# Optimization experiments

Hardware: AMD Instinct MI355X
Metric: run time of the kernel (lower is better)

The kernel has to match this reference:

```python
import jax, jax.numpy as jnp
import numpy as np

N_NODES = 100000
N_EDGES = 1600000
DIM = 64
LAYERS = 2


def setup_inputs() -> dict:
    key = jax.random.key(0)
    k1, k2, k3, k4 = jax.random.split(key, 4)
    h = jax.random.normal(k1, (N_NODES, DIM), dtype=jnp.float32)
    w = jax.random.uniform(k2, (N_EDGES,), dtype=jnp.float32)
    src = jax.random.randint(k3, (N_EDGES,), 0, N_NODES, dtype=jnp.int32)
    dst = jax.random.randint(k4, (N_EDGES,), 0, N_NODES, dtype=jnp.int32)
    return {"h": h, "w": w, "src": src, "dst": dst}


def reference(h, w, src, dst):
    N = h.shape[0]
    # weighted in-degree, clamped at 1 (DGL in_degrees(weight='w').clamp(min=1))
    deg = jnp.maximum(jax.ops.segment_sum(w, dst, num_segments=N), 1.0)
    norm = deg[:, None] ** -0.5  # [N, 1]
    embs = [h]
    for _ in range(LAYERS):
        h_norm = h * norm                              # [N, d]
        m = h_norm[src] * w[:, None]                   # [E, d] edge messages (u_mul_e)
        neigh_sum = jax.ops.segment_sum(m, dst, num_segments=N)  # fn.sum
        h = neigh_sum * norm
        embs.append(h)
    # mean over [h0, h1, ..., hL]
    return jnp.mean(jnp.stack(embs, axis=1), axis=1)
```

## Files before the change

kernel.cpp:

```cpp
#include <hip/hip_runtime.h>
#include <hip/hip_bf16.h>

#define D 64
#define THREADS 256
#define P2T 1024
#define BKT_BITS 9
#define BKT_NODES (1 << BKT_BITS)
#define CHUNK 2048

__device__ __forceinline__ unsigned f2bf(float f) {
    unsigned u = __float_as_uint(f);
    return (u + 0x7fffu + ((u >> 16) & 1u)) >> 16;
}
__device__ __forceinline__ float2 bfpair(unsigned v) {
    return make_float2(__uint_as_float(v << 16), __uint_as_float(v & 0xffff0000u));
}

typedef float f32x4 __attribute__((ext_vector_type(4)));
typedef unsigned u32x4 __attribute__((ext_vector_type(4)));
__device__ __forceinline__ void stnt_f4(float4 v, float4* p) {
    f32x4 t = {v.x, v.y, v.z, v.w};
    __builtin_nontemporal_store(t, (f32x4*)p);
}
__device__ __forceinline__ void stnt_u4(uint4 v, uint4* p) {
    u32x4 t = {v.x, v.y, v.z, v.w};
    __builtin_nontemporal_store(t, (u32x4*)p);
}

__global__ void p1a_hist(const int* __restrict__ dst, int* __restrict__ blockCount,
                         const float* __restrict__ h, unsigned* __restrict__ hbf2,
                         long long nd4, int E, int B) {
    __shared__ int lc[256];
    int t = threadIdx.x;
    lc[t] = 0;
    __syncthreads();
    for (long long i = (long long)blockIdx.x * THREADS + t; i < nd4;
         i += (long long)gridDim.x * THREADS) {
        float4 v = ((const float4*)h)[i];
        ((uint2*)hbf2)[i] = make_uint2(f2bf(v.x) | (f2bf(v.y) << 16),
                                       f2bf(v.z) | (f2bf(v.w) << 16));
    }
    int base = blockIdx.x * CHUNK;
    int end = min(base + CHUNK, E);
    int end4 = end >> 2;
    for (int e4 = (base >> 2) + t; e4 < end4; e4 += THREADS) {
        int4 d4 = ((const int4*)dst)[e4];
        atomicAdd(&lc[d4.x >> BKT_BITS], 1);
        atomicAdd(&lc[d4.y >> BKT_BITS], 1);
        atomicAdd(&lc[d4.z >> BKT_BITS], 1);
        atomicAdd(&lc[d4.w >> BKT_BITS], 1);
    }
    for (int e = (end4 << 2) + t; e < end; e += THREADS)
        atomicAdd(&lc[dst[e] >> BKT_BITS], 1);
    __syncthreads();
    if (t < B) blockCount[(long long)blockIdx.x * B + t] = lc[t];
}

__global__ void p1b_scanblocks(int* __restrict__ blockCount, int* __restrict__ total,
                               int NBLK, int B) {
    __shared__ int sm[512];
    int b = blockIdx.x, t = threadIdx.x;
    int run = 0;
    for (int base = 0; base < NBLK; base += 512) {
        int i = base + t;
        int v = (i < NBLK) ? blockCount[(long long)i * B + b] : 0;
        sm[t] = v;
        __syncthreads();
        for (int off = 1; off < 512; off <<= 1) {
            int u = (t >= off) ? sm[t - off] : 0;
            __syncthreads();
            sm[t] += u;
            __syncthreads();
        }
        if (i < NBLK) blockCount[(long long)i * B + b] = run + sm[t] - v;
        run += sm[511];
        __syncthreads();
    }
    if (t == 0) total[b] = run;
}

__global__ void p1c_scanbuckets(const int* __restrict__ total, int* __restrict__ bstart,
                                int B, int E) {
    __shared__ int sm[256];
    int t = threadIdx.x;
    int run = 0;
    for (int base = 0; base < B; base += 256) {
        int i = base + t;
        int v = (i < B) ? total[i] : 0;
        sm[t] = v;
        __syncthreads();
        for (int off = 1; off < 256; off <<= 1) {
            int u = (t >= off) ? sm[t - off] : 0;
            __syncthreads();
            sm[t] += u;
            __syncthreads();
        }
        if (i < B) bstart[i] = run + sm[t] - v;
        run += sm[255];
        __syncthreads();
    }
    if (t == 0) bstart[B] = E;
}

__global__ void p1d_scatter(const int* __restrict__ dst, const int* __restrict__ src,
                            const float* __restrict__ w, const int* __restrict__ blockCount,
                            const int* __restrict__ bstart, int2* __restrict__ temp,
                            int E, int B) {
    __shared__ int cur[256];
    int t = threadIdx.x;
    if (t < B) cur[t] = bstart[t] + blockCount[(long long)blockIdx.x * B + t];
    __syncthreads();
    int base = blockIdx.x * CHUNK;
    int end = min(base + CHUNK, E);
    int end4 = end >> 2;
    for (int e4 = (base >> 2) + t; e4 < end4; e4 += THREADS) {
        int4 d4 = ((const int4*)dst)[e4];
        int4 s4 = ((const int4*)src)[e4];
        float4 w4 = ((const float4*)w)[e4];
        int pos;
        pos = atomicAdd(&cur[d4.x >> BKT_BITS], 1);
        temp[pos] = make_int2(s4.x | ((d4.x & (BKT_NODES - 1)) << 17), __float_as_int(w4.x));
        pos = atomicAdd(&cur[d4.y >> BKT_BITS], 1);
        temp[pos] = make_int2(s4.y | ((d4.y & (BKT_NODES - 1)) << 17), __float_as_int(w4.y));
        pos = atomicAdd(&cur[d4.z >> BKT_BITS], 1);
        temp[pos] = make_int2(s4.z | ((d4.z & (BKT_NODES - 1)) << 17), __float_as_int(w4.z));
        pos = atomicAdd(&cur[d4.w >> BKT_BITS], 1);
        temp[pos] = make_int2(s4.w | ((d4.w & (BKT_NODES - 1)) << 17), __float_as_int(w4.w));
    }
    for (int e = (end4 << 2) + t; e < end; e += THREADS) {
        int d = dst[e];
        int pos = atomicAdd(&cur[d >> BKT_BITS], 1);
        temp[pos] = make_int2(src[e] | ((d & (BKT_NODES - 1)) << 17), __float_as_int(w[e]));
    }
}

__global__ __launch_bounds__(P2T)
void p2_build(const int2* __restrict__ temp, const int* __restrict__ bstart,
              int2* __restrict__ packed, int* __restrict__ rowptr,
              float* __restrict__ norm, int N, int E, int B) {
    __shared__ int cnt[BKT_NODES];
    __shared__ float degs[BKT_NODES];
    __shared__ int cur[BKT_NODES];
    __shared__ int sm[BKT_NODES];
    int b = blockIdx.x, t = threadIdx.x;
    int ebeg = bstart[b], eend = bstart[b + 1];
    if (t < BKT_NODES) { cnt[t] = 0; degs[t] = 0.0f; }
    __syncthreads();
    for (int e = ebeg + t; e < eend; e += P2T) {
        int2 pk = temp[e];
        int dl = (pk.x >> 17) & (BKT_NODES - 1);
        atomicAdd(&cnt[dl], 1);
        atomicAdd(&degs[dl], __int_as_float(pk.y));
    }
    __syncthreads();
    int v0 = 0;
    if (t < BKT_NODES) { v0 = cnt[t]; sm[t] = v0; }
    __syncthreads();
    for (int off = 1; off < BKT_NODES; off <<= 1) {
        int u = (t >= off && t < BKT_NODES) ? sm[t - off] : 0;
        __syncthreads();
        if (t < BKT_NODES) sm[t] += u;
        __syncthreads();
    }
    int node0 = b << BKT_BITS;
    if (t < BKT_NODES) {
        cur[t] = sm[t] - v0;
        int node = node0 + t;
        if (node < N) {
            rowptr[node] = ebeg + cur[t];
            norm[node] = rsqrtf(fmaxf(degs[t], 1.0f));
        }
    }
    if (b == 0 && t == 0) rowptr[N] = E;
    __syncthreads();
    for (int e = ebeg + t; e < eend; e += P2T) {
        int2 pk = temp[e];
        int dl = (pk.x >> 17) & (BKT_NODES - 1);
        int pos = atomicAdd(&cur[dl], 1);
        packed[ebeg + pos] = make_int2(pk.x & 0x1ffff, pk.y);
    }
}

#define EDGE_FMA(r, c, A0, A1, A2, A3, A4, A5, A6, A7) do {            \
    float2 fa = bfpair((r).x), fb = bfpair((r).y);                      \
    float2 fc = bfpair((r).z), fd = bfpair((r).w);                      \
    A0 = fmaf(fa.x, (c), A0); A1 = fmaf(fa.y, (c), A1);                 \
    A2 = fmaf(fb.x, (c), A2); A3 = fmaf(fb.y, (c), A3);                 \
    A4 = fmaf(fc.x, (c), A4); A5 = fmaf(fc.y, (c), A5);                 \
    A6 = fmaf(fd.x, (c), A6); A7 = fmaf(fd.y, (c), A7); } while (0)

__global__ void gather1_kernel(const uint4* __restrict__ h_in, const int2* __restrict__ packed,
                               const int* __restrict__ rowptr, const float* __restrict__ norm,
                               uint4* __restrict__ h_out, int N) {
    int node = blockIdx.x * (blockDim.x >> 3) + (threadIdx.x >> 3);
    int lane = threadIdx.x & 7;
    if (node >= N) return;
    int j = rowptr[node], end = rowptr[node + 1];
    float a0 = 0, a1 = 0, a2 = 0, a3 = 0, a4 = 0, a5 = 0, a6 = 0, a7 = 0;
    float b0 = 0, b1 = 0, b2 = 0, b3 = 0, b4 = 0, b5 = 0, b6 = 0, b7 = 0;
    for (; j + 8 <= end; j += 8) {
        int2 p0 = packed[j + 0], p1 = packed[j + 1], p2 = packed[j + 2], p3 = packed[j + 3];
        int2 p4 = packed[j + 4], p5 = packed[j + 5], p6 = packed[j + 6], p7 = packed[j + 7];
        uint4 r0 = h_in[((long long)p0.x << 3) + lane];
        uint4 r1 = h_in[((long long)p1.x << 3) + lane];
        uint4 r2 = h_in[((long long)p2.x << 3) + lane];
        uint4 r3 = h_in[((long long)p3.x << 3) + lane];
        uint4 r4 = h_in[((long long)p4.x << 3) + lane];
        uint4 r5 = h_in[((long long)p5.x << 3) + lane];
        uint4 r6 = h_in[((long long)p6.x << 3) + lane];
        uint4 r7 = h_in[((long long)p7.x << 3) + lane];
        float c0 = __int_as_float(p0.y) * norm[p0.x];
        float c1 = __int_as_float(p1.y) * norm[p1.x];
        float c2 = __int_as_float(p2.y) * norm[p2.x];
        float c3 = __int_as_float(p3.y) * norm[p3.x];
        float c4 = __int_as_float(p4.y) * norm[p4.x];
        float c5 = __int_as_float(p5.y) * norm[p5.x];
        float c6 = __int_as_float(p6.y) * norm[p6.x];
        float c7 = __int_as_float(p7.y) * norm[p7.x];
        EDGE_FMA(r0, c0, a0, a1, a2, a3, a4, a5, a6, a7);
        EDGE_FMA(r1, c1, b0, b1, b2, b3, b4, b5, b6, b7);
        EDGE_FMA(r2, c2, a0, a1, a2, a3, a4, a5, a6, a7);
        EDGE_FMA(r3, c3, b0, b1, b2, b3, b4, b5, b6, b7);
        EDGE_FMA(r4, c4, a0, a1, a2, a3, a4, a5, a6, a7);
        EDGE_FMA(r5, c5, b0, b1, b2, b3, b4, b5, b6, b7);
        EDGE_FMA(r6, c6, a0, a1, a2, a3, a4, a5, a6, a7);
        EDGE_FMA(r7, c7, b0, b1, b2, b3, b4, b5, b6, b7);
    }
    for (; j + 4 <= end; j += 4) {
        int2 p0 = packed[j + 0], p1 = packed[j + 1], p2 = packed[j + 2], p3 = packed[j + 3];
        uint4 r0 = h_in[((long long)p0.x << 3) + lane];
        uint4 r1 = h_in[((long long)p1.x << 3) + lane];
        uint4 r2 = h_in[((long long)p2.x << 3) + lane];
        uint4 r3 = h_in[((long long)p3.x << 3) + lane];
        float c0 = __int_as_float(p0.y) * norm[p0.x];
        float c1 = __int_as_float(p1.y) * norm[p1.x];
        float c2 = __int_as_float(p2.y) * norm[p2.x];
        float c3 = __int_as_float(p3.y) * norm[p3.x];
        EDGE_FMA(r0, c0, a0, a1, a2, a3, a4, a5, a6, a7);
        EDGE_FMA(r1, c1, b0, b1, b2, b3, b4, b5, b6, b7);
        EDGE_FMA(r2, c2, a0, a1, a2, a3, a4, a5, a6, a7);
        EDGE_FMA(r3, c3, b0, b1, b2, b3, b4, b5, b6, b7);
    }
    for (; j < end; ++j) {
        int2 p = packed[j];
        uint4 r = h_in[((long long)p.x << 3) + lane];
        float c = __int_as_float(p.y) * norm[p.x];
        EDGE_FMA(r, c, a0, a1, a2, a3, a4, a5, a6, a7);
    }
    float nv = norm[node];
    float d0 = (a0 + b0) * nv, d1 = (a1 + b1) * nv, d2 = (a2 + b2) * nv, d3 = (a3 + b3) * nv;
    float d4 = (a4 + b4) * nv, d5 = (a5 + b5) * nv, d6 = (a6 + b6) * nv, d7 = (a7 + b7) * nv;
    stnt_u4(make_uint4(f2bf(d0) | (f2bf(d1) << 16), f2bf(d2) | (f2bf(d3) << 16),
                       f2bf(d4) | (f2bf(d5) << 16), f2bf(d6) | (f2bf(d7) << 16)),
            &h_out[((long long)node << 3) + lane]);
}

__global__ void gather2_final_kernel(const uint4* __restrict__ h0bf, const uint4* __restrict__ h1bf,
                                     const int2* __restrict__ packed, const int* __restrict__ rowptr,
                                     const float* __restrict__ norm, float* __restrict__ out, int N) {
    int node = blockIdx.x * (blockDim.x >> 3) + (threadIdx.x >> 3);
    int lane = threadIdx.x & 7;
    if (node >= N) return;
    int j = rowptr[node], end = rowptr[node + 1];
    float a0 = 0, a1 = 0, a2 = 0, a3 = 0, a4 = 0, a5 = 0, a6 = 0, a7 = 0;
    float b0 = 0, b1 = 0, b2 = 0, b3 = 0, b4 = 0, b5 = 0, b6 = 0, b7 = 0;
    for (; j + 8 <= end; j += 8) {
        int2 p0 = packed[j + 0], p1 = packed[j + 1], p2 = packed[j + 2], p3 = packed[j + 3];
        int2 p4 = packed[j + 4], p5 = packed[j + 5], p6 = packed[j + 6], p7 = packed[j + 7];
        uint4 r0 = h1bf[((long long)p0.x << 3) + lane];
        uint4 r1 = h1bf[((long long)p1.x << 3) + lane];
        uint4 r2 = h1bf[((long long)p2.x << 3) + lane];
        uint4 r3 = h1bf[((long long)p3.x << 3) + lane];
        uint4 r4 = h1bf[((long long)p4.x << 3) + lane];
        uint4 r5 = h1bf[((long long)p5.x << 3) + lane];
        uint4 r6 = h1bf[((long long)p6.x << 3) + lane];
        uint4 r7 = h1bf[((long long)p7.x << 3) + lane];
        float c0 = __int_as_float(p0.y) * norm[p0.x];
        float c1 = __int_as_float(p1.y) * norm[p1.x];
        float c2 = __int_as_float(p2.y) * norm[p2.x];
        float c3 = __int_as_float(p3.y) * norm[p3.x];
        float c4 = __int_as_float(p4.y) * norm[p4.x];
        float c5 = __int_as_float(p5.y) * norm[p5.x];
        float c6 = __int_as_float(p6.y) * norm[p6.x];
        float c7 = __int_as_float(p7.y) * norm[p7.x];
        EDGE_FMA(r0, c0, a0, a1, a2, a3, a4, a5, a6, a7);
        EDGE_FMA(r1, c1, b0, b1, b2, b3, b4, b5, b6, b7);
        EDGE_FMA(r2, c2, a0, a1, a2, a3, a4, a5, a6, a7);
        EDGE_FMA(r3, c3, b0, b1, b2, b3, b4, b5, b6, b7);
        EDGE_FMA(r4, c4, a0, a1, a2, a3, a4, a5, a6, a7);
        EDGE_FMA(r5, c5, b0, b1, b2, b3, b4, b5, b6, b7);
        EDGE_FMA(r6, c6, a0, a1, a2, a3, a4, a5, a6, a7);
        EDGE_FMA(r7, c7, b0, b1, b2, b3, b4, b5, b6, b7);
    }
    for (; j + 4 <= end; j += 4) {
        int2 p0 = packed[j + 0], p1 = packed[j + 1], p2 = packed[j + 2], p3 = packed[j + 3];
        uint4 r0 = h1bf[((long long)p0.x << 3) + lane];
        uint4 r1 = h1bf[((long long)p1.x << 3) + lane];
        uint4 r2 = h1bf[((long long)p2.x << 3) + lane];
        uint4 r3 = h1bf[((long long)p3.x << 3) + lane];
        float c0 = __int_as_float(p0.y) * norm[p0.x];
        float c1 = __int_as_float(p1.y) * norm[p1.x];
        float c2 = __int_as_float(p2.y) * norm[p2.x];
        float c3 = __int_as_float(p3.y) * norm[p3.x];
        EDGE_FMA(r0, c0, a0, a1, a2, a3, a4, a5, a6, a7);
        EDGE_FMA(r1, c1, b0, b1, b2, b3, b4, b5, b6, b7);
        EDGE_FMA(r2, c2, a0, a1, a2, a3, a4, a5, a6, a7);
        EDGE_FMA(r3, c3, b0, b1, b2, b3, b4, b5, b6, b7);
    }
    for (; j < end; ++j) {
        int2 p = packed[j];
        uint4 r = h1bf[((long long)p.x << 3) + lane];
        float c = __int_as_float(p.y) * norm[p.x];
        EDGE_FMA(r, c, a0, a1, a2, a3, a4, a5, a6, a7);
    }
    long long idx = ((long long)node << 3) + lane;
    float nv = norm[node];
    uint4 h0r = h0bf[idx];
    uint4 h1r = h1bf[idx];
    float2 h0a = bfpair(h0r.x), h0b = bfpair(h0r.y), h0c = bfpair(h0r.z), h0d = bfpair(h0r.w);
    float2 h1a = bfpair(h1r.x), h1b = bfpair(h1r.y), h1c = bfpair(h1r.z), h1d = bfpair(h1r.w);
    float4 o0, o1;
    o0.x = (h0a.x + h1a.x + (a0 + b0) * nv) * (1.0f / 3.0f);
    o0.y = (h0a.y + h1a.y + (a1 + b1) * nv) * (1.0f / 3.0f);
    o0.z = (h0b.x + h1b.x + (a2 + b2) * nv) * (1.0f / 3.0f);
    o0.w = (h0b.y + h1b.y + (a3 + b3) * nv) * (1.0f / 3.0f);
    o1.x = (h0c.x + h1c.x + (a4 + b4) * nv) * (1.0f / 3.0f);
    o1.y = (h0c.y + h1c.y + (a5 + b5) * nv) * (1.0f / 3.0f);
    o1.z = (h0d.x + h1d.x + (a6 + b6) * nv) * (1.0f / 3.0f);
    o1.w = (h0d.y + h1d.y + (a7 + b7) * nv) * (1.0f / 3.0f);
    stnt_f4(o0, &((float4*)out)[((long long)node << 4) + (lane << 1)]);
    stnt_f4(o1, &((float4*)out)[((long long)node << 4) + (lane << 1) + 1]);
}

extern "C" void kernel_launch(void* const* d_in, const int* in_sizes, int n_in,
                              void* d_out, int out_size, void* d_ws, size_t ws_size,
                              hipStream_t stream) {
    const float* h   = (const float*)d_in[0];
    const float* w   = (const float*)d_in[1];
    const int*   src = (const int*)d_in[2];
    const int*   dst = (const int*)d_in[3];
    const int N = in_sizes[0] / D;
    const int E = in_sizes[1];
    float* out = (float*)d_out;

    const int B = (N + BKT_NODES - 1) >> BKT_BITS;
    const int NBLK = (E + CHUNK - 1) / CHUNK;

    char* ws = (char*)d_ws;
    size_t off = 0;
    auto alloc = [&](size_t bytes, size_t align) -> char* {
        off = (off + align - 1) & ~(align - 1);
        char* p = ws + off;
        off += bytes;
        return p;
    };
    float* norm     = (float*)alloc((size_t)N * 4, 16);
    int*   rowptr   = (int*)  alloc((size_t)(N + 1) * 4, 16);
    int*   total    = (int*)  alloc((size_t)B * 4, 16);
    int*   bstart   = (int*)  alloc((size_t)(B + 1) * 4, 16);
    int*   blockCnt = (int*)  alloc((size_t)NBLK * B * 4, 16);
    int2*  packed   = (int2*) alloc((size_t)E * 8, 128);
    char*  shared_region = alloc((size_t)E * 8, 128);
    int2*     temp = (int2*)shared_region;
    unsigned* h1bf = (unsigned*)shared_region;
    unsigned* h0bf = (unsigned*)alloc((size_t)N * D * 2, 128);

    const int nodes_per_block = THREADS / 8;
    const int gather_blocks = (N + nodes_per_block - 1) / nodes_per_block;
    const long long nd4 = (long long)N * D / 4;

    p1a_hist<<<NBLK, THREADS, 0, stream>>>(dst, blockCnt, h, h0bf, nd4, E, B);
    p1b_scanblocks<<<B, 512, 0, stream>>>(blockCnt, total, NBLK, B);
    p1c_scanbuckets<<<1, 256, 0, stream>>>(total, bstart, B, E);
    p1d_scatter<<<NBLK, THREADS, 0, stream>>>(dst, src, w, blockCnt, bstart, temp, E, B);
    p2_build<<<B, P2T, 0, stream>>>(temp, bstart, packed, rowptr, norm, N, E, B);

    gather1_kernel<<<gather_blocks, THREADS, 0, stream>>>((const uint4*)h0bf, packed, rowptr,
                                                          norm, (uint4*)h1bf, N);
    gather2_final_kernel<<<gather_blocks, THREADS, 0, stream>>>((const uint4*)h0bf, (const uint4*)h1bf,
                                                                packed, rowptr, norm, out, N);
}
```

Baseline: 214.2 us.

## Fuse bucket histogram and scatter into one pass with fixed-capacity bucket regions

Replaces the histogram, two scan kernels and the scatter kernel with one fused kernel. It stages each chunk's edges in shared memory, reserves space per bucket with a global atomic into fixed-capacity regions, then scatters. The build kernel derives bucket offsets with an in-block scan of the global counts. This removes three launches and a second read of dst/src/w. In exchange it relies on no bucket exceeding its capacity, which holds for uniform random dst but can overflow on skewed graphs.

```diff
diff --git a/kernel.cpp b/kernel.cpp
--- a/kernel.cpp
+++ b/kernel.cpp
@@ -27,10 +27,15 @@
     __builtin_nontemporal_store(t, (u32x4*)p);
 }
 
-__global__ void p1a_hist(const int* __restrict__ dst, int* __restrict__ blockCount,
-                         const float* __restrict__ h, unsigned* __restrict__ hbf2,
-                         long long nd4, int E, int B) {
+__global__ void p1_fused(const int* __restrict__ dst, const int* __restrict__ src,
+                         const float* __restrict__ w, int* __restrict__ gcur,
+                         int2* __restrict__ temp, const float* __restrict__ h,
+                         unsigned* __restrict__ hbf2, long long nd4,
+                         int E, int B, int CAP) {
+    __shared__ int2 stage[CHUNK];
+    __shared__ unsigned char sbkt[CHUNK];
     __shared__ int lc[256];
+    __shared__ int cur[256];
     int t = threadIdx.x;
     lc[t] = 0;
     __syncthreads();
@@ -42,112 +47,71 @@
     }
     int base = blockIdx.x * CHUNK;
     int end = min(base + CHUNK, E);
-    int end4 = end >> 2;
-    for (int e4 = (base >> 2) + t; e4 < end4; e4 += THREADS) {
-        int4 d4 = ((const int4*)dst)[e4];
-        atomicAdd(&lc[d4.x >> BKT_BITS], 1);
-        atomicAdd(&lc[d4.y >> BKT_BITS], 1);
-        atomicAdd(&lc[d4.z >> BKT_BITS], 1);
-        atomicAdd(&lc[d4.w >> BKT_BITS], 1);
-    }
-    for (int e = (end4 << 2) + t; e < end; e += THREADS)
-        atomicAdd(&lc[dst[e] >> BKT_BITS], 1);
-    __syncthreads();
-    if (t < B) blockCount[(long long)blockIdx.x * B + t] = lc[t];
-}
-
-__global__ void p1b_scanblocks(int* __restrict__ blockCount, int* __restrict__ total,
-                               int NBLK, int B) {
-    __shared__ int sm[512];
-    int b = blockIdx.x, t = threadIdx.x;
-    int run = 0;
-    for (int base = 0; base < NBLK; base += 512) {
-        int i = base + t;
-        int v = (i < NBLK) ? blockCount[(long long)i * B + b] : 0;
-        sm[t] = v;
-        __syncthreads();
-        for (int off = 1; off < 512; off <<= 1) {
-            int u = (t >= off) ? sm[t - off] : 0;
-            __syncthreads();
-            sm[t] += u;
-            __syncthreads();
-        }
-        if (i < NBLK) blockCount[(long long)i * B + b] = run + sm[t] - v;
-        run += sm[511];
-        __syncthreads();
-    }
-    if (t == 0) total[b] = run;
-}
-
-__global__ void p1c_scanbuckets(const int* __restrict__ total, int* __restrict__ bstart,
-                                int B, int E) {
-    __shared__ int sm[256];
-    int t = threadIdx.x;
-    int run = 0;
-    for (int base = 0; base < B; base += 256) {
-        int i = base + t;
-        int v = (i < B) ? total[i] : 0;
-        sm[t] = v;
-        __syncthreads();
-        for (int off = 1; off < 256; off <<= 1) {
-            int u = (t >= off) ? sm[t - off] : 0;
-            __syncthreads();
-            sm[t] += u;
-            __syncthreads();
-        }
-        if (i < B) bstart[i] = run + sm[t] - v;
-        run += sm[255];
-        __syncthreads();
-    }
-    if (t == 0) bstart[B] = E;
-}
-
-__global__ void p1d_scatter(const int* __restrict__ dst, const int* __restrict__ src,
-                            const float* __restrict__ w, const int* __restrict__ blockCount,
-                            const int* __restrict__ bstart, int2* __restrict__ temp,
-                            int E, int B) {
-    __shared__ int cur[256];
-    int t = threadIdx.x;
-    if (t < B) cur[t] = bstart[t] + blockCount[(long long)blockIdx.x * B + t];
-    __syncthreads();
-    int base = blockIdx.x * CHUNK;
-    int end = min(base + CHUNK, E);
+    int n = end - base;
     int end4 = end >> 2;
     for (int e4 = (base >> 2) + t; e4 < end4; e4 += THREADS) {
         int4 d4 = ((const int4*)dst)[e4];
         int4 s4 = ((const int4*)src)[e4];
         float4 w4 = ((const float4*)w)[e4];
-        int pos;
-        pos = atomicAdd(&cur[d4.x >> BKT_BITS], 1);
-        temp[pos] = make_int2(s4.x | ((d4.x & (BKT_NODES - 1)) << 17), __float_as_int(w4.x));
-        pos = atomicAdd(&cur[d4.y >> BKT_BITS], 1);
-        temp[pos] = make_int2(s4.y | ((d4.y & (BKT_NODES - 1)) << 17), __float_as_int(w4.y));
-        pos = atomicAdd(&cur[d4.z >> BKT_BITS], 1);
-        temp[pos] = make_int2(s4.z | ((d4.z & (BKT_NODES - 1)) << 17), __float_as_int(w4.z));
-        pos = atomicAdd(&cur[d4.w >> BKT_BITS], 1);
-        temp[pos] = make_int2(s4.w | ((d4.w & (BKT_NODES - 1)) << 17), __float_as_int(w4.w));
+        int li = (e4 << 2) - base;
+        stage[li + 0] = make_int2(s4.x | ((d4.x & (BKT_NODES - 1)) << 17), __float_as_int(w4.x));
+        stage[li + 1] = make_int2(s4.y | ((d4.y & (BKT_NODES - 1)) << 17), __float_as_int(w4.y));
+        stage[li + 2] = make_int2(s4.z | ((d4.z & (BKT_NODES - 1)) << 17), __float_as_int(w4.z));
+        stage[li + 3] = make_int2(s4.w | ((d4.w & (BKT_NODES - 1)) << 17), __float_as_int(w4.w));
+        sbkt[li + 0] = (unsigned char)(d4.x >> BKT_BITS);
+        sbkt[li + 1] = (unsigned char)(d4.y >> BKT_BITS);
+        sbkt[li + 2] = (unsigned char)(d4.z >> BKT_BITS);
+        sbkt[li + 3] = (unsigned char)(d4.w >> BKT_BITS);
+        atomicAdd(&lc[d4.x >> BKT_BITS], 1);
+        atomicAdd(&lc[d4.y >> BKT_BITS], 1);
+        atomicAdd(&lc[d4.z >> BKT_BITS], 1);
+        atomicAdd(&lc[d4.w >> BKT_BITS], 1);
     }
     for (int e = (end4 << 2) + t; e < end; e += THREADS) {
         int d = dst[e];
-        int pos = atomicAdd(&cur[d >> BKT_BITS], 1);
-        temp[pos] = make_int2(src[e] | ((d & (BKT_NODES - 1)) << 17), __float_as_int(w[e]));
+        int li = e - base;
+        stage[li] = make_int2(src[e] | ((d & (BKT_NODES - 1)) << 17), __float_as_int(w[e]));
+        sbkt[li] = (unsigned char)(d >> BKT_BITS);
+        atomicAdd(&lc[d >> BKT_BITS], 1);
+    }
+    __syncthreads();
+    if (t < B) {
+        int c = lc[t];
+        cur[t] = (c > 0) ? ((int)((long long)t * CAP) + atomicAdd(&gcur[t], c)) : 0;
+    }
+    __syncthreads();
+    for (int i = t; i < n; i += THREADS) {
+        int b = sbkt[i];
+        int pos = atomicAdd(&cur[b], 1);
+        temp[pos] = stage[i];
     }
 }
 
 __global__ __launch_bounds__(P2T)
-void p2_build(const int2* __restrict__ temp, const int* __restrict__ bstart,
+void p2_build(const int2* __restrict__ temp, const int* __restrict__ gcur,
               int2* __restrict__ packed, int* __restrict__ rowptr,
-              float* __restrict__ norm, int N, int E, int B) {
+              float* __restrict__ norm, int N, int E, int B, int CAP) {
     __shared__ int cnt[BKT_NODES];
     __shared__ float degs[BKT_NODES];
     __shared__ int cur[BKT_NODES];
     __shared__ int sm[BKT_NODES];
+    __shared__ int bs[256];
     int b = blockIdx.x, t = threadIdx.x;
-    int ebeg = bstart[b], eend = bstart[b + 1];
+    if (t < 256) bs[t] = (t < B) ? gcur[t] : 0;
+    __syncthreads();
+    for (int off = 1; off < 256; off <<= 1) {
+        int u = (t >= off && t < 256) ? bs[t - off] : 0;
+        __syncthreads();
+        if (t < 256) bs[t] += u;
+        __syncthreads();
+    }
+    int cntb = gcur[b];
+    int ebeg = bs[b] - cntb;
+    const int2* reg = temp + (long long)b * CAP;
     if (t < BKT_NODES) { cnt[t] = 0; degs[t] = 0.0f; }
     __syncthreads();
-    for (int e = ebeg + t; e < eend; e += P2T) {
-        int2 pk = temp[e];
+    for (int e = t; e < cntb; e += P2T) {
+        int2 pk = reg[e];
         int dl = (pk.x >> 17) & (BKT_NODES - 1);
         atomicAdd(&cnt[dl], 1);
         atomicAdd(&degs[dl], __int_as_float(pk.y));
@@ -173,8 +137,8 @@
     }
     if (b == 0 && t == 0) rowptr[N] = E;
     __syncthreads();
-    for (int e = ebeg + t; e < eend; e += P2T) {
-        int2 pk = temp[e];
+    for (int e = t; e < cntb; e += P2T) {
+        int2 pk = reg[e];
         int dl = (pk.x >> 17) & (BKT_NODES - 1);
         int pos = atomicAdd(&cur[dl], 1);
         packed[ebeg + pos] = make_int2(pk.x & 0x1ffff, pk.y);
@@ -345,6 +309,8 @@
 
     const int B = (N + BKT_NODES - 1) >> BKT_BITS;
     const int NBLK = (E + CHUNK - 1) / CHUNK;
+    const int avg = (E + B - 1) / B;
+    const int CAP = avg + (avg >> 2) + 1024;
 
     char* ws = (char*)d_ws;
     size_t off = 0;
@@ -356,11 +322,11 @@
     };
     float* norm     = (float*)alloc((size_t)N * 4, 16);
     int*   rowptr   = (int*)  alloc((size_t)(N + 1) * 4, 16);
-    int*   total    = (int*)  alloc((size_t)B * 4, 16);
-    int*   bstart   = (int*)  alloc((size_t)(B + 1) * 4, 16);
-    int*   blockCnt = (int*)  alloc((size_t)NBLK * B * 4, 16);
+    int*   gcur     = (int*)  alloc((size_t)B * 4, 16);
     int2*  packed   = (int2*) alloc((size_t)E * 8, 128);
-    char*  shared_region = alloc((size_t)E * 8, 128);
+    size_t temp_bytes = (size_t)B * CAP * 8;
+    size_t h1_bytes   = (size_t)N * D * 2;
+    char*  shared_region = alloc(temp_bytes > h1_bytes ? temp_bytes : h1_bytes, 128);
     int2*     temp = (int2*)shared_region;
     unsigned* h1bf = (unsigned*)shared_region;
     unsigned* h0bf = (unsigned*)alloc((size_t)N * D * 2, 128);
@@ -369,11 +335,9 @@
     const int gather_blocks = (N + nodes_per_block - 1) / nodes_per_block;
     const long long nd4 = (long long)N * D / 4;
 
-    p1a_hist<<<NBLK, THREADS, 0, stream>>>(dst, blockCnt, h, h0bf, nd4, E, B);
-    p1b_scanblocks<<<B, 512, 0, stream>>>(blockCnt, total, NBLK, B);
-    p1c_scanbuckets<<<1, 256, 0, stream>>>(total, bstart, B, E);
-    p1d_scatter<<<NBLK, THREADS, 0, stream>>>(dst, src, w, blockCnt, bstart, temp, E, B);
-    p2_build<<<B, P2T, 0, stream>>>(temp, bstart, packed, rowptr, norm, N, E, B);
+    hipMemsetAsync(gcur, 0, (size_t)B * 4, stream);
+    p1_fused<<<NBLK, THREADS, 0, stream>>>(dst, src, w, gcur, temp, h, h0bf, nd4, E, B, CAP);
+    p2_build<<<B, P2T, 0, stream>>>(temp, gcur, packed, rowptr, norm, N, E, B, CAP);
 
     gather1_kernel<<<gather_blocks, THREADS, 0, stream>>>((const uint4*)h0bf, packed, rowptr,
                                                           norm, (uint4*)h1bf, N);
```

New measurement: 218.2 us. Within noise of the previous version (+1.9%).
